# Kernel optimization log

Measured on AMD Instinct MI355X. Metric: run time of the kernel, lower is better.

The kernel has to match this reference:

```python
import jax, jax.numpy as jnp
import numpy as np

N_QUBITS = 8
TRASH = 1
DEPTH = 2
DIM = 2 ** N_QUBITS  # 256

# Qiskit little-endian: amplitude index k has qubit 0 as LSB. Reshaping a
# 256-vector to (2,)*8 puts qubit (N-1-a) on tensor axis a (axis 0 = MSB).
# Observable j is SparsePauliOp with 'Z' at string pos j => Z on qubit N-1-j
# => tensor axis j. So exp_j = sum probs * (1 - 2*bit_axis_j).


def _rx(t):
    c = jnp.cos(t / 2).astype(jnp.complex64)
    ms = (-1j * jnp.sin(t / 2)).astype(jnp.complex64)
    return jnp.stack([jnp.stack([c, ms]), jnp.stack([ms, c])])


def _ry(t):
    c = jnp.cos(t / 2).astype(jnp.complex64)
    s = jnp.sin(t / 2).astype(jnp.complex64)
    return jnp.stack([jnp.stack([c, -s]), jnp.stack([s, c])])


def _rz(t):
    e = jnp.exp((-0.5j) * t.astype(jnp.complex64))
    z = jnp.zeros_like(e)
    return jnp.stack([jnp.stack([e, z]), jnp.stack([z, jnp.conj(e)])])


def _apply_1q(psi, U, q):
    ax = 1 + (N_QUBITS - 1 - q)
    return jnp.moveaxis(jnp.tensordot(psi, U, axes=([ax], [1])), -1, ax)


def _apply_cx(psi, c, t):
    axc = 1 + (N_QUBITS - 1 - c)
    axt = 1 + (N_QUBITS - 1 - t)
    shape = [1] * psi.ndim
    shape[axc] = 2
    ctrl = (jnp.arange(2).reshape(shape) == 1)
    return jnp.where(ctrl, jnp.flip(psi, axis=axt), psi)


def _r3_ansatz(psi, theta, nq, depth):
    k = 0
    for _ in range(depth):
        for q in range(nq):
            psi = _apply_1q(psi, _rx(theta[k + 0]), q)
            psi = _apply_1q(psi, _ry(theta[k + 1]), q)
            psi = _apply_1q(psi, _rz(theta[k + 2]), q)
            k += 3
        for q in range(nq - 1):  # linear entanglement
            psi = _apply_cx(psi, q, q + 1)
    return psi


# sign matrix for Z expectations: S[j, k] = 1 - 2*bit_{N-1-j}(k)
_k = np.arange(DIM)
_SIGNS = np.stack([1.0 - 2.0 * ((_k >> (N_QUBITS - 1 - j)) & 1)
                   for j in range(N_QUBITS)]).astype(np.float32)  # (8, 256)


def setup_inputs() -> dict:
    key = jax.random.key(0)
    k1, k2, k3, k4 = jax.random.split(key, 4)
    return {
        "x": jax.random.normal(k1, (32, 1024, 256), dtype=jnp.float32),
        "theta1": jax.random.normal(k2, (DEPTH * N_QUBITS * 3,), dtype=jnp.float32),
        "theta2": jax.random.normal(k3, (DEPTH * (N_QUBITS - TRASH) * 3,), dtype=jnp.float32),
        "theta3": jax.random.normal(k4, (DEPTH * N_QUBITS * 3,), dtype=jnp.float32),
    }


def reference(x, theta1, theta2, theta3):
    B, T, D = x.shape
    xf = x.reshape(B * T, D)
    # amplitude encode: normalize classical vector into quantum amplitudes
    norm = jnp.linalg.norm(xf, axis=1, keepdims=True)
    norm = jnp.where(norm == 0, jnp.float32(1e-8), norm)
    psi = (xf / norm).astype(jnp.complex64).reshape((B * T,) + (2,) * N_QUBITS)
    # ansatz: U1 (8q) -> U2 (7q) -> U3 (8q)
    psi = _r3_ansatz(psi, theta1, N_QUBITS, DEPTH)
    psi = _r3_ansatz(psi, theta2, N_QUBITS - TRASH, DEPTH)
    psi = _r3_ansatz(psi, theta3, N_QUBITS, DEPTH)
    # Z expectation on each observable
    probs = (jnp.abs(psi) ** 2).reshape(B * T, DIM)
    y = probs @ jnp.asarray(_SIGNS).T  # (B*T, 8)
    # amplitude decode: normalize, |.|^2, zero-pad to DIM
    yn = jnp.linalg.norm(y, axis=1, keepdims=True)
    yn = jnp.where(yn == 0, jnp.float32(1e-8), yn)
    cv = (y / yn) ** 2
    out = jnp.pad(cv, ((0, 0), (0, DIM - N_QUBITS)))
    return out.reshape(B, T, DIM)
```

## Files before the change

kernel.cpp:

```cpp
#include <hip/hip_runtime.h>
#include <math.h>


#define DEV __device__ __forceinline__

typedef __attribute__((ext_vector_type(8))) short short8;
typedef __attribute__((ext_vector_type(4))) float f32x4;

DEV float2 cmul(float2 a, float2 b) {
  return make_float2(a.x * b.x - a.y * b.y, a.x * b.y + a.y * b.x);
}
DEV float2 cadd(float2 a, float2 b) { return make_float2(a.x + b.x, a.y + b.y); }

DEV unsigned short bf_rne(float v) {
  unsigned u = __float_as_uint(v);
  return (unsigned short)((u + 0x7FFFu + ((u >> 16) & 1u)) >> 16);
}


struct Psi4 { float re[4]; float im[4]; };

template <int Q>
DEV void pair_gate(Psi4& s, const float2* __restrict__ Mlo,
                   const float2* __restrict__ Mhi, int lane) {
  const int b0 = (lane >> Q) & 1, b1 = (lane >> (Q + 1)) & 1;
  float2 lo_d = Mlo[b0 * 2 + b0];
  float2 lo_o = Mlo[b0 * 2 + (b0 ^ 1)];
  float2 hi_d = Mhi[b1 * 2 + b1];
  float2 hi_o = Mhi[b1 * 2 + (b1 ^ 1)];
  float2 c00 = cmul(hi_d, lo_d);
  float2 c01 = cmul(hi_d, lo_o);
  float2 c10 = cmul(hi_o, lo_d);
  float2 c11 = cmul(hi_o, lo_o);
  const int m0 = 1 << Q, m1 = 2 << Q;
#pragma unroll
  for (int r = 0; r < 4; ++r) {
    float ar = s.re[r], ai = s.im[r];
    float p0r = __shfl_xor(ar, m0, 64), p0i = __shfl_xor(ai, m0, 64);
    float p1r = __shfl_xor(ar, m1, 64), p1i = __shfl_xor(ai, m1, 64);
    float p2r = __shfl_xor(ar, m0 | m1, 64), p2i = __shfl_xor(ai, m0 | m1, 64);
    float nr = c00.x * ar - c00.y * ai + c01.x * p0r - c01.y * p0i
             + c10.x * p1r - c10.y * p1i + c11.x * p2r - c11.y * p2i;
    float ni = c00.x * ai + c00.y * ar + c01.x * p0i + c01.y * p0r
             + c10.x * p1i + c10.y * p1r + c11.x * p2i + c11.y * p2r;
    s.re[r] = nr; s.im[r] = ni;
  }
}

DEV void regpair_gate(Psi4& s, const float2* __restrict__ Mlo,
                      const float2* __restrict__ Mhi) {
  float nr[4], ni[4];
#pragma unroll
  for (int r = 0; r < 4; ++r) {
    const int b0 = r & 1, b1 = (r >> 1) & 1;
    float2 c00 = cmul(Mhi[b1 * 2 + b1], Mlo[b0 * 2 + b0]);
    float2 c01 = cmul(Mhi[b1 * 2 + b1], Mlo[b0 * 2 + (b0 ^ 1)]);
    float2 c10 = cmul(Mhi[b1 * 2 + (b1 ^ 1)], Mlo[b0 * 2 + b0]);
    float2 c11 = cmul(Mhi[b1 * 2 + (b1 ^ 1)], Mlo[b0 * 2 + (b0 ^ 1)]);
    nr[r] = c00.x * s.re[r] - c00.y * s.im[r]
          + c01.x * s.re[r ^ 1] - c01.y * s.im[r ^ 1]
          + c10.x * s.re[r ^ 2] - c10.y * s.im[r ^ 2]
          + c11.x * s.re[r ^ 3] - c11.y * s.im[r ^ 3];
    ni[r] = c00.x * s.im[r] + c00.y * s.re[r]
          + c01.x * s.im[r ^ 1] + c01.y * s.re[r ^ 1]
          + c10.x * s.im[r ^ 2] + c10.y * s.re[r ^ 2]
          + c11.x * s.im[r ^ 3] + c11.y * s.re[r ^ 3];
  }
#pragma unroll
  for (int r = 0; r < 4; ++r) { s.re[r] = nr[r]; s.im[r] = ni[r]; }
}

DEV void reg0_gate(Psi4& s, const float2* __restrict__ M) {
  float nr[4], ni[4];
#pragma unroll
  for (int r = 0; r < 4; ++r) {
    const int b = r & 1;
    float2 d = M[b * 2 + b], o = M[b * 2 + (b ^ 1)];
    nr[r] = d.x * s.re[r] - d.y * s.im[r] + o.x * s.re[r ^ 1] - o.y * s.im[r ^ 1];
    ni[r] = d.x * s.im[r] + d.y * s.re[r] + o.x * s.im[r ^ 1] + o.y * s.re[r ^ 1];
  }
#pragma unroll
  for (int r = 0; r < 4; ++r) { s.re[r] = nr[r]; s.im[r] = ni[r]; }
}

template <bool FULL8>
DEV void perm_cx(Psi4& s, int lane) {
  const int slane = (lane ^ (lane << 1)) & 63;
  const bool L5 = ((lane >> 5) & 1) != 0;
  float nr[4], ni[4];
#pragma unroll
  for (int r = 0; r < 4; ++r) {
    const int r0 = r & 1, r1 = (r >> 1) & 1;
    const int hiBit = FULL8 ? (r1 ^ r0) : r1;
    const int sA = (hiBit << 1) | r0;
    const int sB = sA ^ 1;
    float aRe = __shfl(s.re[sA], slane, 64);
    float aIm = __shfl(s.im[sA], slane, 64);
    float bRe = __shfl(s.re[sB], slane, 64);
    float bIm = __shfl(s.im[sB], slane, 64);
    nr[r] = L5 ? bRe : aRe;
    ni[r] = L5 ? bIm : aIm;
  }
#pragma unroll
  for (int r = 0; r < 4; ++r) { s.re[r] = nr[r]; s.im[r] = ni[r]; }
}

template <int NQ>
DEV void ansatz_f(Psi4& s, const float2* __restrict__ Mg, int lane) {
#pragma unroll
  for (int d = 0; d < 2; ++d) {
    const float2* Md = Mg + d * NQ * 4;
    pair_gate<0>(s, Md + 0, Md + 4, lane);
    pair_gate<2>(s, Md + 8, Md + 12, lane);
    pair_gate<4>(s, Md + 16, Md + 20, lane);
    if (NQ == 8) regpair_gate(s, Md + 24, Md + 28);
    else reg0_gate(s, Md + 24);
    perm_cx<NQ == 8>(s, lane);
  }
}

DEV void store_v(unsigned short* __restrict__ Vsw, int n, int kk, float v) {
  int k = kk >> 5, rem = kk & 31, quad = rem >> 3, jj = rem & 7;
  int nn = n & 255;
  int w = (nn >> 6) & 3, t = (nn >> 4) & 3, cl = nn & 15;
  int g = w * 8 + ((n >= 256) ? 4 + t : t);
  int L = quad * 16 + cl;
  unsigned short hi = bf_rne(v);
  float hif = __uint_as_float(((unsigned)hi) << 16);
  unsigned short lo = bf_rne(v - hif);
  size_t base = (size_t)k * 32768 + (size_t)g * 1024 + (size_t)L * 8 + jj;
  Vsw[base] = hi;
  Vsw[base + 512] = lo;
}

__global__ void build_u(const float* __restrict__ th1, const float* __restrict__ th2,
                        const float* __restrict__ th3, unsigned short* __restrict__ Vsw) {
  __shared__ float2 Mg[46 * 4];
  const int tid = threadIdx.x;
  if (tid < 46) {
    float thx, thy, thz;
    if (tid < 16)      { thx = th1[tid * 3]; thy = th1[tid * 3 + 1]; thz = th1[tid * 3 + 2]; }
    else if (tid < 30) { int u = (tid - 16) * 3; thx = th2[u]; thy = th2[u + 1]; thz = th2[u + 2]; }
    else               { int u = (tid - 30) * 3; thx = th3[u]; thy = th3[u + 1]; thz = th3[u + 2]; }
    float sx, cx_, sy, cy_, sz, cz_;
    sincosf(0.5f * thx, &sx, &cx_);
    sincosf(0.5f * thy, &sy, &cy_);
    sincosf(0.5f * thz, &sz, &cz_);
    float2 rx[4] = {{cx_, 0}, {0, -sx}, {0, -sx}, {cx_, 0}};
    float2 ry[4] = {{cy_, 0}, {-sy, 0}, {sy, 0}, {cy_, 0}};
    float2 A0 = cadd(cmul(ry[0], rx[0]), cmul(ry[1], rx[2]));
    float2 A1 = cadd(cmul(ry[0], rx[1]), cmul(ry[1], rx[3]));
    float2 A2 = cadd(cmul(ry[2], rx[0]), cmul(ry[3], rx[2]));
    float2 A3 = cadd(cmul(ry[2], rx[1]), cmul(ry[3], rx[3]));
    float2 ezm = make_float2(cz_, -sz), ezp = make_float2(cz_, sz);
    Mg[tid * 4 + 0] = cmul(ezm, A0);
    Mg[tid * 4 + 1] = cmul(ezm, A1);
    Mg[tid * 4 + 2] = cmul(ezp, A2);
    Mg[tid * 4 + 3] = cmul(ezp, A3);
  }
  __syncthreads();

  const int lane = tid & 63;
  const int j = blockIdx.x * 4 + (tid >> 6);
  Psi4 s;
#pragma unroll
  for (int r = 0; r < 4; ++r) {
    int a = (r << 6) | lane;
    s.re[r] = (a == j) ? 1.f : 0.f;
    s.im[r] = 0.f;
  }
  ansatz_f<8>(s, Mg, lane);
  ansatz_f<7>(s, Mg + 16 * 4, lane);
  ansatz_f<8>(s, Mg + 30 * 4, lane);
#pragma unroll
  for (int r = 0; r < 4; ++r) {
    int a = (r << 6) | lane;
    store_v(Vsw, a, j, s.re[r]);
    store_v(Vsw, a + 256, j, s.im[r]);
  }
}


__global__ __launch_bounds__(512, 2) void pqc_main(const float* __restrict__ x,
                                                   const unsigned short* __restrict__ Vsw,
                                                   float* __restrict__ out) {
  const int tid = threadIdx.x;
  const int ww = tid >> 6;
  const int w = ww >> 1;
  const int half = ww & 1;
  const int L = tid & 63;
  const int quad = L >> 4;
  const int c = L & 15;
  const int row0 = blockIdx.x * 128;

  __shared__ unsigned short A2[2][8][8][512];
  __shared__ float ys[128][8];
  __shared__ float invn[128];
  float* part = (float*)&A2[0][0][0][0];

  {
    const float4* xsrc = (const float4*)(x + (size_t)row0 * 256);
#pragma unroll
    for (int i = 0; i < 16; ++i) {
      int e = i * 512 + tid;
      int row = e >> 6;
      int kk = (e & 63) * 4;
      float4 f = xsrc[e];
      ushort4 h, l;
#define SPLIT1(fld, v)                                           \
      {                                                          \
        unsigned u = __float_as_uint(v);                         \
        h.fld = (unsigned short)(u >> 16);         \
        float hf = __uint_as_float(u & 0xFFFF0000u);             \
        l.fld = (unsigned short)(__float_as_uint((v) - hf) >> 16); \
      }
      SPLIT1(x, f.x) SPLIT1(y, f.y) SPLIT1(z, f.z) SPLIT1(w, f.w)
#undef SPLIT1
      int mt = row >> 4, cc = row & 15;
      int k = kk >> 5, q = (kk >> 3) & 3, j = kk & 7;
      int idx = (q * 16 + cc) * 8 + j;
      *(ushort4*)&A2[0][k][mt][idx] = h;
      *(ushort4*)&A2[1][k][mt][idx] = l;
    }
  }
  __syncthreads();

  f32x4 acc[8][4];
#pragma unroll
  for (int mt = 0; mt < 8; ++mt)
#pragma unroll
    for (int tt = 0; tt < 4; ++tt) acc[mt][tt] = (f32x4){0.f, 0.f, 0.f, 0.f};

  const unsigned short* pb = Vsw + (size_t)w * 8192 + (size_t)half * 4096 + (size_t)L * 8;

#pragma unroll 1
  for (int k = 0; k < 8; ++k) {
    short8 ah[8], al[8];
#pragma unroll
    for (int mt = 0; mt < 8; ++mt) {
      ah[mt] = *(const short8*)&A2[0][k][mt][L * 8];
      al[mt] = *(const short8*)&A2[1][k][mt][L * 8];
    }
    const unsigned short* pk = pb + (size_t)k * 32768;
#pragma unroll
    for (int tt = 0; tt < 4; ++tt) {
      short8 bh = *(const short8*)(pk + tt * 1024);
      short8 bl = *(const short8*)(pk + tt * 1024 + 512);
#pragma unroll
      for (int mt = 0; mt < 8; ++mt)
        acc[mt][tt] = __builtin_amdgcn_mfma_f32_16x16x32_bf16(ah[mt], bh, acc[mt][tt], 0, 0, 0);
#pragma unroll
      for (int mt = 0; mt < 8; ++mt)
        acc[mt][tt] = __builtin_amdgcn_mfma_f32_16x16x32_bf16(al[mt], bh, acc[mt][tt], 0, 0, 0);
#pragma unroll
      for (int mt = 0; mt < 8; ++mt)
        acc[mt][tt] = __builtin_amdgcn_mfma_f32_16x16x32_bf16(ah[mt], bl, acc[mt][tt], 0, 0, 0);
    }
  }
  __syncthreads();

#pragma unroll
  for (int mt = 0; mt < 8; ++mt) {
#pragma unroll
    for (int r = 0; r < 4; ++r) {
      float p0 = acc[mt][0][r] * acc[mt][0][r];
      float p1 = acc[mt][1][r] * acc[mt][1][r];
      float p2 = acc[mt][2][r] * acc[mt][2][r];
      float p3 = acc[mt][3][r] * acc[mt][3][r];
      float s01 = p0 + p1, s23 = p2 + p3;
      float av = s01 + s23;
      float bv = s01 - s23;
      float cv = (p0 - p1) + (p2 - p3);
#pragma unroll
      for (int st = 0; st < 4; ++st) {
        int msk = 1 << st;
        float ta = __shfl_xor(av, msk, 64);
        av = ((c >> st) & 1) ? (ta - av) : (av + ta);
        bv += __shfl_xor(bv, msk, 64);
        cv += __shfl_xor(cv, msk, 64);
      }
      int m = mt * 16 + quad * 4 + r;
      float* pm = part + (ww * 128 + m) * 8;
      if (c == 0) {
        pm[0] = ((w >> 1) & 1) ? -av : av;
        pm[1] = (w & 1) ? -av : av;
        pm[2] = bv;
        pm[3] = cv;
      } else if (c == 8) pm[4] = av;
      else if (c == 4) pm[5] = av;
      else if (c == 2) pm[6] = av;
      else if (c == 1) pm[7] = av;
    }
  }
  __syncthreads();

#pragma unroll
  for (int s = 0; s < 2; ++s) {
    int e = s * 512 + tid;
    int m = e >> 3, jj = e & 7;
    float acc_y = 0.f;
#pragma unroll
    for (int p = 0; p < 8; ++p) acc_y += part[(p * 128 + m) * 8 + jj];
    ys[m][jj] = acc_y;
  }
  __syncthreads();

  if (tid < 128) {
    float n = 0.f;
#pragma unroll
    for (int jj = 0; jj < 8; ++jj) { float v = ys[tid][jj]; n = fmaf(v, v, n); }
    n = sqrtf(n);
    invn[tid] = (n == 0.f) ? 0.f : 1.f / n;
  }
  __syncthreads();

  float4* o4 = (float4*)(out + (size_t)row0 * 256);
#pragma unroll
  for (int i = 0; i < 16; ++i) {
    int e = i * 512 + tid;
    int row = e >> 6;
    int c4 = (e & 63) * 4;
    float4 v = make_float4(0.f, 0.f, 0.f, 0.f);
    if (c4 < 8) {
      float iv = invn[row];
      float t0 = ys[row][c4 + 0] * iv;
      float t1 = ys[row][c4 + 1] * iv;
      float t2 = ys[row][c4 + 2] * iv;
      float t3 = ys[row][c4 + 3] * iv;
      v = make_float4(t0 * t0, t1 * t1, t2 * t2, t3 * t3);
    }
    o4[e] = v;
  }
}

extern "C" void kernel_launch(void* const* d_in, const int* in_sizes, int n_in,
                              void* d_out, int out_size, void* d_ws, size_t ws_size,
                              hipStream_t stream) {
  const float* x = (const float*)d_in[0];
  const float* th1 = (const float*)d_in[1];
  const float* th2 = (const float*)d_in[2];
  const float* th3 = (const float*)d_in[3];
  float* out = (float*)d_out;
  unsigned short* Vsw = (unsigned short*)d_ws;

  build_u<<<64, 256, 0, stream>>>(th1, th2, th3, Vsw);
  pqc_main<<<256, 512, 0, stream>>>(x, Vsw, out);
}
```

Baseline: 126.2 us.

## Swizzle A tile LDS layout, remap x loads, use DPP for butterfly reductions

Remaps the global load of x so each wave fills one k-slice of the LDS A tile, and XOR-swizzles the row index within that tile to cut LDS bank conflicts on both the stores and the MFMA operand reads. The 16-lane butterfly reductions in the epilogue move from __shfl_xor, which goes through ds_bpermute, to DPP row moves with sign-bit masking in place of the select. This trades some register and instruction changes for fewer LDS round trips, and correctness depends on the DPP controls matching the xor patterns.

```diff
diff --git a/kernel.cpp b/kernel.cpp
--- a/kernel.cpp
+++ b/kernel.cpp
@@ -16,6 +16,16 @@
   unsigned u = __float_as_uint(v);
   return (unsigned short)((u + 0x7FFFu + ((u >> 16) & 1u)) >> 16);
 }
+
+template <int CTRL>
+DEV float dppf(float v) {
+  return __int_as_float(__builtin_amdgcn_mov_dpp(__float_as_int(v), CTRL, 0xF, 0xF, true));
+}
+DEV float px1(float v) { return dppf<0xB1>(v); }
+DEV float px2(float v) { return dppf<0x4E>(v); }
+DEV float px4(float v) { return dppf<0x1B>(dppf<0x141>(v)); }
+DEV float px8(float v) { return dppf<0x141>(dppf<0x140>(v)); }
+DEV float fsgn(float v, int m) { return __int_as_float(__float_as_int(v) ^ m); }
 
 
 struct Psi4 { float re[4]; float im[4]; };
@@ -200,12 +210,14 @@
 
   {
     const float4* xsrc = (const float4*)(x + (size_t)row0 * 256);
+    const int r8 = L & 7;
+    const int kf = L >> 3;
+    const int q = kf >> 1;
+    const int jj0 = (kf & 1) * 4;
 #pragma unroll
     for (int i = 0; i < 16; ++i) {
-      int e = i * 512 + tid;
-      int row = e >> 6;
-      int kk = (e & 63) * 4;
-      float4 f = xsrc[e];
+      int row = i * 8 + r8;
+      float4 f = xsrc[row * 64 + ww * 8 + kf];
       ushort4 h, l;
 #define SPLIT1(fld, v)                                           \
       {                                                          \
@@ -217,10 +229,9 @@
       SPLIT1(x, f.x) SPLIT1(y, f.y) SPLIT1(z, f.z) SPLIT1(w, f.w)
 #undef SPLIT1
       int mt = row >> 4, cc = row & 15;
-      int k = kk >> 5, q = (kk >> 3) & 3, j = kk & 7;
-      int idx = (q * 16 + cc) * 8 + j;
-      *(ushort4*)&A2[0][k][mt][idx] = h;
-      *(ushort4*)&A2[1][k][mt][idx] = l;
+      int idx = (q * 16 + (cc ^ (q << 1))) * 8 + jj0;
+      *(ushort4*)&A2[0][ww][mt][idx] = h;
+      *(ushort4*)&A2[1][ww][mt][idx] = l;
     }
   }
   __syncthreads();
@@ -232,14 +243,15 @@
     for (int tt = 0; tt < 4; ++tt) acc[mt][tt] = (f32x4){0.f, 0.f, 0.f, 0.f};
 
   const unsigned short* pb = Vsw + (size_t)w * 8192 + (size_t)half * 4096 + (size_t)L * 8;
+  const int sL8 = (quad * 16 + (c ^ (quad << 1))) * 8;
 
 #pragma unroll 1
   for (int k = 0; k < 8; ++k) {
     short8 ah[8], al[8];
 #pragma unroll
     for (int mt = 0; mt < 8; ++mt) {
-      ah[mt] = *(const short8*)&A2[0][k][mt][L * 8];
-      al[mt] = *(const short8*)&A2[1][k][mt][L * 8];
+      ah[mt] = *(const short8*)&A2[0][k][mt][sL8];
+      al[mt] = *(const short8*)&A2[1][k][mt][sL8];
     }
     const unsigned short* pk = pb + (size_t)k * 32768;
 #pragma unroll
@@ -259,6 +271,10 @@
   }
   __syncthreads();
 
+  const int m1 = (c & 1) << 31;
+  const int m2 = (c & 2) << 30;
+  const int m4 = (c & 4) << 29;
+  const int m8 = (c & 8) << 28;
 #pragma unroll
   for (int mt = 0; mt < 8; ++mt) {
 #pragma unroll
@@ -271,14 +287,14 @@
       float av = s01 + s23;
       float bv = s01 - s23;
       float cv = (p0 - p1) + (p2 - p3);
-#pragma unroll
-      for (int st = 0; st < 4; ++st) {
-        int msk = 1 << st;
-        float ta = __shfl_xor(av, msk, 64);
-        av = ((c >> st) & 1) ? (ta - av) : (av + ta);
-        bv += __shfl_xor(bv, msk, 64);
-        cv += __shfl_xor(cv, msk, 64);
-      }
+      av = px1(av) + fsgn(av, m1);
+      bv += px1(bv);  cv += px1(cv);
+      av = px2(av) + fsgn(av, m2);
+      bv += px2(bv);  cv += px2(cv);
+      av = px4(av) + fsgn(av, m4);
+      bv += px4(bv);  cv += px4(cv);
+      av = px8(av) + fsgn(av, m8);
+      bv += px8(bv);  cv += px8(cv);
       int m = mt * 16 + quad * 4 + r;
       float* pm = part + (ww * 128 + m) * 8;
       if (c == 0) {
```

Result: faster. 122.6 us (-2.8%).
